# Kernel tuning notes

Measured on AMD Instinct MI355X. Metric: run time of the kernel, lower is better.

## Reference

```python
import jax, jax.numpy as jnp
import numpy as np

B, C, H, W = 2, 48, 64, 64
EPS = 1e-5
ROW = [0, 0, 0, H // 4, H // 4, H // 4, H // 2, H // 2, H // 2]
COL = [0, W // 4, W // 2] * 3


def setup_inputs() -> dict:
    key = jax.random.key(0)
    ks = iter(jax.random.split(key, 40))
    s = 1.0 / np.sqrt(C)  # keep unscaled-softmax logits sane
    def rn(shape, scale=1.0):
        return jax.random.normal(next(ks), shape, jnp.float32) * scale
    def ru(shape):
        return jax.random.uniform(next(ks), shape, jnp.float32, 0.5, 1.5)
    return dict(
        input_feature=rn((B, C, H, W)), feat_b=rn((B, C, H, W)),
        feat_c=rn((B, C, H, W)), feat_d=rn((B, C, H, W)),
        W_fa_all=rn((C, C), s), W_fb_all=rn((C, C), s),
        W_fc_all=rn((C, C), s), W_fd_all=rn((C, C), s),
        W_fa=rn((9, C, C), s), W_fb=rn((9, C, C), s),
        W_fc=rn((9, C, C), s), W_fd=rn((9, C, C), s),
        fuse_w=rn((C, 4 * C), s), fuse_b=rn((C,), 0.1),
        fuse_g=ru((C,)), fuse_bb=rn((C,), 0.1), fuse_m=rn((C,), 0.1), fuse_v=ru((C,)),
        fuseP_w=rn((9, C, 4 * C), s), fuseP_b=rn((9, C), 0.1),
        fuseP_g=ru((9, C)), fuseP_bb=rn((9, C), 0.1), fuseP_m=rn((9, C), 0.1), fuseP_v=ru((9, C)),
        gamma_all=rn(()), gamma_p=rn((9,)),
        out_w=rn((C, C, 3, 3), s / 3.0), out_b=rn((C,), 0.1),
        out_g=ru((C,)), out_bb=rn((C,), 0.1), out_m=rn((C,), 0.1), out_v=ru((C,)),
    )


def _attn(q, k, v):
    # q,k,v: [..., C, N] -> energy [..., N, N]; non-standard softmax(max - energy)
    e = jnp.einsum('...cn,...cm->...nm', q, k)
    e = jnp.max(e, axis=-1, keepdims=True) - e
    a = jax.nn.softmax(e, axis=-1)
    return jnp.einsum('...cn,...nm->...cm', v, a)  # torch.matmul(v, attention)


def reference(input_feature, feat_b, feat_c, feat_d,
              W_fa_all, W_fb_all, W_fc_all, W_fd_all,
              W_fa, W_fb, W_fc, W_fd,
              fuse_w, fuse_b, fuse_g, fuse_bb, fuse_m, fuse_v,
              fuseP_w, fuseP_b, fuseP_g, fuseP_bb, fuseP_m, fuseP_v,
              gamma_all, gamma_p,
              out_w, out_b, out_g, out_bb, out_m, out_v):
    h2, w2 = H // 2, W // 2
    N = H * W
    # ---- global branch: channel-wise Linear (bias=False) applied over spatial tokens
    fa = jnp.einsum('dc,bcn->bdn', W_fa_all, input_feature.reshape(B, C, N))
    fb = jnp.einsum('dc,bcn->bdn', W_fb_all, feat_b.reshape(B, C, N))
    fc = jnp.einsum('dc,bcn->bdn', W_fc_all, feat_c.reshape(B, C, N))
    fd = jnp.einsum('dc,bcn->bdn', W_fd_all, feat_d.reshape(B, C, N))
    cat = jnp.concatenate([_attn(fa, fa, fa), _attn(fa, fb, fb),
                           _attn(fa, fc, fc), _attn(fa, fd, fd)], axis=1)
    cat = cat.reshape(B, 4 * C, H, W)
    y = jnp.einsum('oc,bchw->bohw', fuse_w, cat) + fuse_b[None, :, None, None]
    y = (y - fuse_m[:, None, None]) * (fuse_g / jnp.sqrt(fuse_v + EPS))[:, None, None] + fuse_bb[:, None, None]
    atten_all = jax.nn.relu(y)  # Dropout2d is identity at eval
    # ---- 9 overlapping patch branches, vectorized over the patch axis p
    def crops(x):
        return jnp.stack([x[:, :, r:r + h2, c:c + w2] for r, c in zip(ROW, COL)], 0).reshape(9, B, C, h2 * w2)
    pa = jnp.einsum('pdc,pbcn->pbdn', W_fa, crops(input_feature))
    pb = jnp.einsum('pdc,pbcn->pbdn', W_fb, crops(feat_b))
    pc = jnp.einsum('pdc,pbcn->pbdn', W_fc, crops(feat_c))
    pd = jnp.einsum('pdc,pbcn->pbdn', W_fd, crops(feat_d))
    pcat = jnp.concatenate([_attn(pa, pa, pa), _attn(pa, pb, pb),
                            _attn(pa, pc, pc), _attn(pa, pd, pd)], axis=2)
    pcat = pcat.reshape(9, B, 4 * C, h2, w2)
    py = jnp.einsum('poc,pbchw->pbohw', fuseP_w, pcat) + fuseP_b[:, None, :, None, None]
    py = ((py - fuseP_m[:, None, :, None, None])
          * (fuseP_g / jnp.sqrt(fuseP_v + EPS))[:, None, :, None, None]
          + fuseP_bb[:, None, :, None, None])
    patch_out = 0.5 * gamma_p[:, None, None, None, None] * jax.nn.relu(py)
    # ---- combine (overlapping patch regions accumulate additively, as in torch +=)
    out = input_feature + gamma_all * atten_all
    for i, (r, c) in enumerate(zip(ROW, COL)):
        out = out.at[:, :, r:r + h2, c:c + w2].add(patch_out[i])
    # ---- to_out: 3x3 conv + BN(eval) + ReLU
    z = jax.lax.conv_general_dilated(out, out_w, (1, 1), 'SAME',
                                     dimension_numbers=('NCHW', 'OIHW', 'NCHW'))
    z = z + out_b[None, :, None, None]
    z = (z - out_m[:, None, None]) * (out_g / jnp.sqrt(out_v + EPS))[:, None, None] + out_bb[:, None, None]
    return jax.nn.relu(z)
```

## Files before the change

kernel.cpp:

```cpp
#include <hip/hip_runtime.h>
#include <math.h>

typedef _Float16 f16;
typedef f16 f16x8 __attribute__((ext_vector_type(8)));
typedef float f32x4 __attribute__((ext_vector_type(4)));

namespace {
constexpr int B_ = 2, C_ = 48, H_ = 64, W_ = 64;
constexpr int N_ = H_ * W_;
constexpr int NP_ = 1024;
constexpr int C4_ = 4 * C_;
constexpr float EPS_ = 1e-5f;
constexpr float L2E_ = 1.44269504f;
constexpr float REFL2_ = -25.0f * 1.44269504f;
}

#define MFMA32(a, b, c) __builtin_amdgcn_mfma_f32_16x16x32_f16((a), (b), (c), 0, 0, 0)

__device__ inline float fast_exp2(float x) {
#if __has_builtin(__builtin_amdgcn_exp2f)
  return __builtin_amdgcn_exp2f(x);
#else
  float r;
  asm("v_exp_f32 %0, %1" : "=v"(r) : "v"(x));
  return r;
#endif
}

__device__ __attribute__((always_inline)) void proj_body(
    const float* __restrict__ xb, const float* __restrict__ Ws,
    f16* __restrict__ pnb, size_t pn_stride, f16* __restrict__ ptb) {
  float acc[48];
#pragma unroll
  for (int d = 0; d < 48; ++d) acc[d] = 0.f;
  for (int c0 = 0; c0 < 48; c0 += 4) {
    float xv0 = xb[(size_t)(c0 + 0) * 4096];
    float xv1 = xb[(size_t)(c0 + 1) * 4096];
    float xv2 = xb[(size_t)(c0 + 2) * 4096];
    float xv3 = xb[(size_t)(c0 + 3) * 4096];
#pragma unroll
    for (int d = 0; d < 48; ++d) {
      const float4 wv = *(const float4*)&Ws[d * 48 + c0];
      acc[d] = fmaf(wv.x, xv0, fmaf(wv.y, xv1, fmaf(wv.z, xv2, fmaf(wv.w, xv3, acc[d]))));
    }
  }
#pragma unroll
  for (int d = 0; d < 48; ++d) pnb[(size_t)d * pn_stride] = (f16)acc[d];
#pragma unroll
  for (int s = 0; s < 6; ++s) {
    f16x8 v;
#pragma unroll
    for (int j = 0; j < 8; ++j) v[j] = (f16)acc[s * 8 + j];
    *(f16x8*)(ptb + s * 8) = v;
  }
  f16x8 zv = {0, 0, 0, 0, 0, 0, 0, 0};
  *(f16x8*)(ptb + 48) = zv;
  *(f16x8*)(ptb + 56) = zv;
}

__global__ __launch_bounds__(256) void k_proj_all(
    const float* __restrict__ x0, const float* __restrict__ x1,
    const float* __restrict__ x2, const float* __restrict__ x3,
    const float* __restrict__ w0, const float* __restrict__ w1,
    const float* __restrict__ w2, const float* __restrict__ w3,
    const float* __restrict__ wp0, const float* __restrict__ wp1,
    const float* __restrict__ wp2, const float* __restrict__ wp3,
    f16* __restrict__ pgn, f16* __restrict__ pgt,
    f16* __restrict__ ppn, f16* __restrict__ ppt) {
  __shared__ float Ws[48 * 48];
  int tid = threadIdx.x;
  int bid = blockIdx.x;
  if (bid < 128) {
    int bx = bid & 15, b = (bid >> 4) & 1, X = bid >> 5;
    const float* xp = X == 0 ? x0 : X == 1 ? x1 : X == 2 ? x2 : x3;
    const float* wp = X == 0 ? w0 : X == 1 ? w1 : X == 2 ? w2 : w3;
    for (int i = tid; i < 2304; i += 256) Ws[i] = wp[i];
    __syncthreads();
    int n = bx * 256 + tid;
    int z2 = X * 2 + b;
    proj_body(xp + (size_t)b * 48 * 4096 + n, Ws,
              pgn + ((size_t)z2 * 48) * 4096 + n, 4096,
              pgt + ((size_t)z2 * 4096 + n) * 64);
  } else {
    int pid = bid - 128;
    int bx = pid & 3;
    int rest = pid >> 2;
    int p = rest % 9;
    int zb = rest / 9;
    int X = zb >> 1, b = zb & 1;
    const float* xp = X == 0 ? x0 : X == 1 ? x1 : X == 2 ? x2 : x3;
    const float* wp = (X == 0 ? wp0 : X == 1 ? wp1 : X == 2 ? wp2 : wp3) + (size_t)p * 2304;
    for (int i = tid; i < 2304; i += 256) Ws[i] = wp[i];
    __syncthreads();
    int t = bx * 256 + tid;
    int r0 = (p / 3) * 16, c0w = (p % 3) * 16;
    int rr = r0 + (t >> 5), cc = c0w + (t & 31);
    int z9 = (X * 2 + b) * 9 + p;
    proj_body(xp + (size_t)b * 48 * 4096 + rr * 64 + cc, Ws,
              ppn + ((size_t)z9 * 48) * 1024 + t, 1024,
              ppt + ((size_t)z9 * 1024 + t) * 64);
  }
}

template <int NT, int NSPLIT, bool PATCH>
__device__ __attribute__((always_inline)) void stats_body(
    const f16* __restrict__ qT_all, const f16* __restrict__ kT_all,
    float* __restrict__ stp, int bx, int by, uint4* Ks) {
  constexpr int MTI = (NT / NSPLIT) / 64;
  int tid = threadIdx.x, wave = tid >> 6, lane = tid & 63, g = lane >> 4, lm = lane & 15;
  int ms = by % NSPLIT, z = by / NSPLIT;
  const f16* qT;
  if (PATCH) {
    int b = (z / 9) % 2, p = z % 9;
    qT = qT_all + ((size_t)(b * 9 + p)) * NT * 64;
  } else {
    int b = z & 1;
    qT = qT_all + (size_t)b * NT * 64;
  }
  const f16* kT = kT_all + (size_t)z * NT * 64;
  int n0 = bx * 128 + wave * 16;
  f16x8 aq0a = *(const f16x8*)(qT + (size_t)(n0 + lm) * 64 + g * 8);
  f16x8 aq1a = *(const f16x8*)(qT + (size_t)(n0 + lm) * 64 + 32 + g * 8);
  f16x8 aq0b = *(const f16x8*)(qT + (size_t)(n0 + 64 + lm) * 64 + g * 8);
  f16x8 aq1b = *(const f16x8*)(qT + (size_t)(n0 + 64 + lm) * 64 + 32 + g * 8);
  const int s0r = tid >> 3, s0c = (tid & 7) * 8;
  const int sw0 = tid ^ ((tid >> 3) & 7);
  const int sw1 = (tid + 256) ^ (((tid + 256) >> 3) & 7);
  const int swl = lm & 7;
  const int c0i = g ^ swl, c1i = (4 + g) ^ swl;
  int t_beg = ms * MTI;
  {
    const f16* src = kT + (size_t)t_beg * 64 * 64;
    Ks[sw0] = *(const uint4*)(src + (size_t)s0r * 64 + s0c);
    Ks[sw1] = *(const uint4*)(src + (size_t)(s0r + 32) * 64 + s0c);
  }
  __syncthreads();
  float zsa[4] = {0.f, 0.f, 0.f, 0.f};
  float zsb[4] = {0.f, 0.f, 0.f, 0.f};
  for (int mt = 0; mt < MTI; ++mt) {
    int cur = mt & 1;
    bool pf = (mt + 1 < MTI);
    uint4 k0v, k1v;
    if (pf) {
      const f16* src = kT + (size_t)(t_beg + mt + 1) * 64 * 64;
      k0v = *(const uint4*)(src + (size_t)s0r * 64 + s0c);
      k1v = *(const uint4*)(src + (size_t)(s0r + 32) * 64 + s0c);
    }
    uint4* kb = Ks + cur * 512;
    __builtin_amdgcn_s_setprio(1);
#pragma unroll
    for (int mf = 0; mf < 4; ++mf) {
      f16x8 b0 = __builtin_bit_cast(f16x8, kb[(16 * mf + lm) * 8 + c0i]);
      f16x8 b1 = __builtin_bit_cast(f16x8, kb[(16 * mf + lm) * 8 + c1i]);
      f32x4 ea = {0.f, 0.f, 0.f, 0.f};
      ea = MFMA32(aq0a, b0, ea);
      ea = MFMA32(aq1a, b1, ea);
      f32x4 eb = {0.f, 0.f, 0.f, 0.f};
      eb = MFMA32(aq0b, b0, eb);
      eb = MFMA32(aq1b, b1, eb);
#pragma unroll
      for (int r = 0; r < 4; ++r) {
        zsa[r] += fast_exp2(fmaf(ea[r], -L2E_, REFL2_));
        zsb[r] += fast_exp2(fmaf(eb[r], -L2E_, REFL2_));
      }
    }
    __builtin_amdgcn_s_setprio(0);
    if (pf) {
      uint4* kn = Ks + (cur ^ 1) * 512;
      kn[sw0] = k0v;
      kn[sw1] = k1v;
    }
    __syncthreads();
  }
#pragma unroll
  for (int mask = 1; mask < 16; mask <<= 1) {
#pragma unroll
    for (int r = 0; r < 4; ++r) {
      zsa[r] += __shfl_xor(zsa[r], mask, 64);
      zsb[r] += __shfl_xor(zsb[r], mask, 64);
    }
  }
  if (lm == 0) {
#pragma unroll
    for (int r = 0; r < 4; ++r) {
      stp[((size_t)z * NT + n0 + 4 * g + r) * NSPLIT + ms] = zsa[r];
      stp[((size_t)z * NT + n0 + 64 + 4 * g + r) * NSPLIT + ms] = zsb[r];
    }
  }
}

__global__ __launch_bounds__(256, 6) void k_stats_all(
    const f16* __restrict__ pg_t, float* __restrict__ stpg,
    const f16* __restrict__ pp_t, float* __restrict__ stpp) {
  __shared__ uint4 Ks[2 * 512];
  int bid = blockIdx.x;
  if (bid < 1024) {
    stats_body<N_, 4, false>(pg_t, pg_t, stpg, bid & 31, bid >> 5, Ks);
  } else {
    int pid = bid - 1024;
    stats_body<NP_, 1, true>(pp_t, pp_t, stpp, pid & 7, pid >> 3, Ks);
  }
}

__global__ __launch_bounds__(256) void k_merge_all(
    const float* __restrict__ stpg, float* __restrict__ stg,
    const float* __restrict__ stpp, float* __restrict__ stp2) {
  int i = blockIdx.x * 256 + threadIdx.x;
  if (i < 8 * N_) {
    const float* p = stpg + (size_t)i * 4;
    float Z = p[0] + p[1] + p[2] + p[3];
    stg[i] = REFL2_ - __log2f(Z);
  } else {
    int j = i - 8 * N_;
    if (j < 72 * NP_) stp2[j] = REFL2_ - __log2f(stpp[j]);
  }
}

template <int NT, int NSPLIT, bool PATCH>
__device__ __attribute__((always_inline)) void pv_body(
    const f16* __restrict__ qT_all, const f16* __restrict__ kT_all,
    const f16* __restrict__ vN_all, const float* __restrict__ st_all,
    float* __restrict__ out_all, int bx, int by,
    float* As2, uint4* Qs, uint4* Vs, uint2* wt2) {
  constexpr int CH = NT / NSPLIT;
  constexpr int NTI = CH / 64;
  int tid = threadIdx.x, wave = tid >> 6, lane = tid & 63, g = lane >> 4, lm = lane & 15;
  int ns = by % NSPLIT, z = by / NSPLIT;
  const f16 *qT, *kT, *vN;
  float* op;
  if (PATCH) {
    int X = z / 18, b = (z / 9) % 2, p = z % 9;
    qT = qT_all + ((size_t)(b * 9 + p)) * NT * 64;
    op = out_all + ((size_t)((p * 2 + b) * C4_ + X * 48)) * NT;
  } else {
    int X = z >> 1, b = z & 1;
    qT = qT_all + (size_t)b * NT * 64;
    op = out_all + ((size_t)(b * C4_ + X * 48)) * NT;
  }
  kT = kT_all + (size_t)z * NT * 64;
  vN = vN_all + (size_t)z * 48 * NT;
  const float* st = st_all + (size_t)z * NT + ns * CH;
  ((float4*)As2)[tid] = ((const float4*)st)[tid];
  int mwa = bx * 128 + wave * 16;
  int mwb = mwa + 64;
  f16x8 bk0a = *(const f16x8*)(kT + (size_t)(mwa + lm) * 64 + g * 8);
  f16x8 bk1a = *(const f16x8*)(kT + (size_t)(mwa + lm) * 64 + 32 + g * 8);
  f16x8 bk0b = *(const f16x8*)(kT + (size_t)(mwb + lm) * 64 + g * 8);
  f16x8 bk1b = *(const f16x8*)(kT + (size_t)(mwb + lm) * 64 + 32 + g * 8);
  const int s0r = tid >> 3, s0c = (tid & 7) * 8;
  const int sw0 = tid ^ ((tid >> 3) & 7);
  const int sw1 = (tid + 256) ^ (((tid + 256) >> 3) & 7);
  const int swl = lm & 7;
  const int c0i = g ^ swl, c1i = (4 + g) ^ swl;
  int t_beg = ns * NTI;
  {
    const f16* qsrc = qT + (size_t)t_beg * 64 * 64;
    Qs[sw0] = *(const uint4*)(qsrc + (size_t)s0r * 64 + s0c);
    Qs[sw1] = *(const uint4*)(qsrc + (size_t)(s0r + 32) * 64 + s0c);
    Vs[sw0] = *(const uint4*)(vN + (size_t)s0r * NT + t_beg * 64 + s0c);
    if (tid < 128)
      Vs[sw1] = *(const uint4*)(vN + (size_t)(s0r + 32) * NT + t_beg * 64 + s0c);
  }
  __syncthreads();
  f32x4 oa0 = {0.f, 0.f, 0.f, 0.f}, oa1 = {0.f, 0.f, 0.f, 0.f}, oa2 = {0.f, 0.f, 0.f, 0.f};
  f32x4 ob0 = {0.f, 0.f, 0.f, 0.f}, ob1 = {0.f, 0.f, 0.f, 0.f}, ob2 = {0.f, 0.f, 0.f, 0.f};
  int wbufa = wave * 512;
  int wbufb = wave * 512 + 256;
  int rba = wbufa + lm * 16;
  int rbb = wbufb + lm * 16;
  for (int nt = 0; nt < NTI; ++nt) {
    bool pf = (nt + 1 < NTI);
    uint4 q0v, q1v, v0v, v1v;
    if (pf) {
      int tn = t_beg + nt + 1;
      const f16* qsrc = qT + (size_t)tn * 64 * 64;
      q0v = *(const uint4*)(qsrc + (size_t)s0r * 64 + s0c);
      q1v = *(const uint4*)(qsrc + (size_t)(s0r + 32) * 64 + s0c);
      v0v = *(const uint4*)(vN + (size_t)s0r * NT + tn * 64 + s0c);
      if (tid < 128)
        v1v = *(const uint4*)(vN + (size_t)(s0r + 32) * NT + tn * 64 + s0c);
    }
    f32x4 ea[4], eb[4];
    __builtin_amdgcn_s_setprio(1);
#pragma unroll
    for (int nf = 0; nf < 4; ++nf) {
      f16x8 a0 = __builtin_bit_cast(f16x8, Qs[(16 * nf + lm) * 8 + c0i]);
      f16x8 a1 = __builtin_bit_cast(f16x8, Qs[(16 * nf + lm) * 8 + c1i]);
      f32x4 ta = {0.f, 0.f, 0.f, 0.f};
      ta = MFMA32(a0, bk0a, ta);
      ta = MFMA32(a1, bk1a, ta);
      ea[nf] = ta;
      f32x4 tb = {0.f, 0.f, 0.f, 0.f};
      tb = MFMA32(a0, bk0b, tb);
      tb = MFMA32(a1, bk1b, tb);
      eb[nf] = tb;
    }
    __builtin_amdgcn_s_setprio(0);
#pragma unroll
    for (int nf = 0; nf < 4; ++nf) {
      float4 a4 = *(const float4*)&As2[nt * 64 + nf * 16 + g * 4];
      float wa0 = fast_exp2(fmaf(ea[nf][0], -L2E_, a4.x));
      float wa1 = fast_exp2(fmaf(ea[nf][1], -L2E_, a4.y));
      float wa2 = fast_exp2(fmaf(ea[nf][2], -L2E_, a4.z));
      float wa3 = fast_exp2(fmaf(ea[nf][3], -L2E_, a4.w));
      float wb0 = fast_exp2(fmaf(eb[nf][0], -L2E_, a4.x));
      float wb1 = fast_exp2(fmaf(eb[nf][1], -L2E_, a4.y));
      float wb2 = fast_exp2(fmaf(eb[nf][2], -L2E_, a4.z));
      float wb3 = fast_exp2(fmaf(eb[nf][3], -L2E_, a4.w));
      unsigned la = __builtin_bit_cast(unsigned, __builtin_amdgcn_cvt_pkrtz(wa0, wa1));
      unsigned ha = __builtin_bit_cast(unsigned, __builtin_amdgcn_cvt_pkrtz(wa2, wa3));
      unsigned lb = __builtin_bit_cast(unsigned, __builtin_amdgcn_cvt_pkrtz(wb0, wb1));
      unsigned hb = __builtin_bit_cast(unsigned, __builtin_amdgcn_cvt_pkrtz(wb2, wb3));
      int s = 2 * nf + (g >> 1);
      int so = ((s ^ swl) * 2) + (g & 1);
      wt2[wbufa + lm * 16 + so] = make_uint2(la, ha);
      wt2[wbufb + lm * 16 + so] = make_uint2(lb, hb);
    }
    __builtin_amdgcn_sched_barrier(0);
    f16x8 bw0a = __builtin_bit_cast(f16x8, *(const uint4*)&wt2[rba + c0i * 2]);
    f16x8 bw1a = __builtin_bit_cast(f16x8, *(const uint4*)&wt2[rba + c1i * 2]);
    f16x8 bw0b = __builtin_bit_cast(f16x8, *(const uint4*)&wt2[rbb + c0i * 2]);
    f16x8 bw1b = __builtin_bit_cast(f16x8, *(const uint4*)&wt2[rbb + c1i * 2]);
    __builtin_amdgcn_s_setprio(1);
#pragma unroll
    for (int cf = 0; cf < 3; ++cf) {
      f16x8 av0 = __builtin_bit_cast(f16x8, Vs[(16 * cf + lm) * 8 + c0i]);
      f16x8 av1 = __builtin_bit_cast(f16x8, Vs[(16 * cf + lm) * 8 + c1i]);
      if (cf == 0) {
        oa0 = MFMA32(av0, bw0a, oa0); oa0 = MFMA32(av1, bw1a, oa0);
        ob0 = MFMA32(av0, bw0b, ob0); ob0 = MFMA32(av1, bw1b, ob0);
      }
      if (cf == 1) {
        oa1 = MFMA32(av0, bw0a, oa1); oa1 = MFMA32(av1, bw1a, oa1);
        ob1 = MFMA32(av0, bw0b, ob1); ob1 = MFMA32(av1, bw1b, ob1);
      }
      if (cf == 2) {
        oa2 = MFMA32(av0, bw0a, oa2); oa2 = MFMA32(av1, bw1a, oa2);
        ob2 = MFMA32(av0, bw0b, ob2); ob2 = MFMA32(av1, bw1b, ob2);
      }
    }
    __builtin_amdgcn_s_setprio(0);
    __syncthreads();
    if (pf) {
      Qs[sw0] = q0v;
      Qs[sw1] = q1v;
      Vs[sw0] = v0v;
      if (tid < 128) Vs[sw1] = v1v;
    }
    __syncthreads();
  }
  if (NSPLIT == 1) {
#pragma unroll
    for (int r = 0; r < 4; ++r) {
      op[(size_t)(0 + 4 * g + r) * NT + mwa + lm] = oa0[r];
      op[(size_t)(16 + 4 * g + r) * NT + mwa + lm] = oa1[r];
      op[(size_t)(32 + 4 * g + r) * NT + mwa + lm] = oa2[r];
      op[(size_t)(0 + 4 * g + r) * NT + mwb + lm] = ob0[r];
      op[(size_t)(16 + 4 * g + r) * NT + mwb + lm] = ob1[r];
      op[(size_t)(32 + 4 * g + r) * NT + mwb + lm] = ob2[r];
    }
  } else {
#pragma unroll
    for (int r = 0; r < 4; ++r) {
      atomicAdd(&op[(size_t)(0 + 4 * g + r) * NT + mwa + lm], oa0[r]);
      atomicAdd(&op[(size_t)(16 + 4 * g + r) * NT + mwa + lm], oa1[r]);
      atomicAdd(&op[(size_t)(32 + 4 * g + r) * NT + mwa + lm], oa2[r]);
      atomicAdd(&op[(size_t)(0 + 4 * g + r) * NT + mwb + lm], ob0[r]);
      atomicAdd(&op[(size_t)(16 + 4 * g + r) * NT + mwb + lm], ob1[r]);
      atomicAdd(&op[(size_t)(32 + 4 * g + r) * NT + mwb + lm], ob2[r]);
    }
  }
}

__global__ __launch_bounds__(256, 4) void k_pv_all(
    const f16* __restrict__ pg_t, const f16* __restrict__ pg_n,
    const float* __restrict__ statsg, float* __restrict__ cat,
    const f16* __restrict__ pp_t, const f16* __restrict__ pp_n,
    const float* __restrict__ statsp, float* __restrict__ pcat) {
  __shared__ float As2[1024];
  __shared__ uint4 Qs[512];
  __shared__ uint4 Vs[384];
  __shared__ uint2 wt2[2048];
  int bid = blockIdx.x;
  if (bid < 1024) {
    pv_body<N_, 4, false>(pg_t, pg_t, pg_n, statsg, cat, bid & 31, bid >> 5,
                          As2, Qs, Vs, wt2);
  } else {
    int pid = bid - 1024;
    pv_body<NP_, 1, true>(pp_t, pp_t, pp_n, statsp, pcat, pid & 7, pid >> 3,
                          As2, Qs, Vs, wt2);
  }
}

__global__ __launch_bounds__(256) void k_fuse_all(
    const float* __restrict__ cat, const float* __restrict__ fw,
    const float* __restrict__ fb, const float* __restrict__ fg,
    const float* __restrict__ fbb, const float* __restrict__ fm,
    const float* __restrict__ fv, const float* __restrict__ gamma_all,
    const float* __restrict__ input, float* __restrict__ comb,
    const float* __restrict__ pcat, const float* __restrict__ pfw,
    const float* __restrict__ pfb, const float* __restrict__ pfg,
    const float* __restrict__ pfbb, const float* __restrict__ pfm,
    const float* __restrict__ pfv, const float* __restrict__ gamma_p) {
  int bid = blockIdx.x;
  if (bid < 384) {
    int idx = bid * 256 + threadIdx.x;
    int n4 = idx & 1023;
    int rest = idx >> 10;
    int o = rest % C_;
    int b = rest / C_;
    const float* cr = cat + (size_t)b * C4_ * N_ + n4 * 4;
    const float* wr = fw + (size_t)o * C4_;
    float4 acc = {0.f, 0.f, 0.f, 0.f};
#pragma unroll 8
    for (int c = 0; c < C4_; ++c) {
      float4 xv = *(const float4*)(cr + (size_t)c * N_);
      float w = wr[c];
      acc.x = fmaf(w, xv.x, acc.x); acc.y = fmaf(w, xv.y, acc.y);
      acc.z = fmaf(w, xv.z, acc.z); acc.w = fmaf(w, xv.w, acc.w);
    }
    float scale = fg[o] * rsqrtf(fv[o] + EPS_);
    float sh = fb[o] - fm[o], bb = fbb[o], ga = gamma_all[0];
    float4 inv = *(const float4*)(input + ((size_t)(b * C_ + o) * N_) + n4 * 4);
    float* base = comb + ((size_t)(b * C_ + o) * N_) + n4 * 4;
    atomicAdd(base + 0, inv.x + ga * fmaxf((acc.x + sh) * scale + bb, 0.f));
    atomicAdd(base + 1, inv.y + ga * fmaxf((acc.y + sh) * scale + bb, 0.f));
    atomicAdd(base + 2, inv.z + ga * fmaxf((acc.z + sh) * scale + bb, 0.f));
    atomicAdd(base + 3, inv.w + ga * fmaxf((acc.w + sh) * scale + bb, 0.f));
  } else {
    int idx = (bid - 384) * 256 + threadIdx.x;
    int t4 = idx & 255;
    int rest = idx >> 8;
    int o = rest % C_; rest /= C_;
    int b = rest % B_;
    int p = rest / B_;
    const float* cr = pcat + ((size_t)(p * B_ + b) * C4_) * NP_ + t4 * 4;
    const float* wr = pfw + (size_t)(p * C_ + o) * C4_;
    float4 acc = {0.f, 0.f, 0.f, 0.f};
#pragma unroll 8
    for (int c = 0; c < C4_; ++c) {
      float4 xv = *(const float4*)(cr + (size_t)c * NP_);
      float w = wr[c];
      acc.x = fmaf(w, xv.x, acc.x); acc.y = fmaf(w, xv.y, acc.y);
      acc.z = fmaf(w, xv.z, acc.z); acc.w = fmaf(w, xv.w, acc.w);
    }
    int po = p * C_ + o;
    float scale = pfg[po] * rsqrtf(pfv[po] + EPS_);
    float sh = pfb[po] - pfm[po], bb = pfbb[po], gp = 0.5f * gamma_p[p];
    int t = t4 * 4;
    int r0 = (p / 3) * 16, c0w = (p % 3) * 16;
    int h = r0 + (t >> 5), w = c0w + (t & 31);
    float* base = comb + ((size_t)(b * C_ + o) * N_) + h * 64 + w;
    atomicAdd(base + 0, gp * fmaxf((acc.x + sh) * scale + bb, 0.f));
    atomicAdd(base + 1, gp * fmaxf((acc.y + sh) * scale + bb, 0.f));
    atomicAdd(base + 2, gp * fmaxf((acc.z + sh) * scale + bb, 0.f));
    atomicAdd(base + 3, gp * fmaxf((acc.w + sh) * scale + bb, 0.f));
  }
}

__global__ __launch_bounds__(256) void k_conv2(
    const float* __restrict__ comb, const float* __restrict__ cw,
    const float* __restrict__ cb, const float* __restrict__ cg,
    const float* __restrict__ cbb, const float* __restrict__ cm,
    const float* __restrict__ cv, float* __restrict__ out) {
  __shared__ float4 inh[4608];
  int tid = threadIdx.x;
  int h0 = blockIdx.x * 4, ocg = blockIdx.y, b = blockIdx.z;
  for (int i = tid; i < 4608; i += 256) {
    int c = i / 96;
    int rem = i - c * 96;
    int r = rem >> 4, u = rem & 15;
    int hh = h0 - 1 + r;
    float4 val = make_float4(0.f, 0.f, 0.f, 0.f);
    if (hh >= 0 && hh < H_)
      val = *(const float4*)(comb + (((size_t)(b * C_ + c) * H_ + hh) * W_ + u * 4));
    inh[i] = val;
  }
  __syncthreads();
  int w = tid & 63, dh = tid >> 6;
  float acc[6] = {0.f, 0.f, 0.f, 0.f, 0.f, 0.f};
  const float* lds = (const float*)inh;
  int wm = w > 0 ? w - 1 : 0;
  int wp = w < 63 ? w + 1 : 63;
  for (int c = 0; c < 48; ++c) {
    float v[9];
#pragma unroll
    for (int r = 0; r < 3; ++r) {
      const float* row = lds + (size_t)(c * 6 + dh + r) * 64;
      float lf = row[wm];
      float md = row[w];
      float rt = row[wp];
      v[r * 3 + 0] = (w > 0) ? lf : 0.f;
      v[r * 3 + 1] = md;
      v[r * 3 + 2] = (w < 63) ? rt : 0.f;
    }
#pragma unroll
    for (int j = 0; j < 6; ++j) {
      const float* wr = cw + (size_t)((ocg * 6 + j) * 48 + c) * 9;
#pragma unroll
      for (int k = 0; k < 9; ++k) acc[j] = fmaf(v[k], wr[k], acc[j]);
    }
  }
#pragma unroll
  for (int j = 0; j < 6; ++j) {
    int o = ocg * 6 + j;
    float scale = cg[o] * rsqrtf(cv[o] + EPS_);
    float y = (acc[j] + cb[o] - cm[o]) * scale + cbb[o];
    out[(size_t)(b * C_ + o) * N_ + (h0 + dh) * 64 + w] = fmaxf(y, 0.f);
  }
}

extern "C" void kernel_launch(void* const* d_in, const int* in_sizes, int n_in,
                              void* d_out, int out_size, void* d_ws, size_t ws_size,
                              hipStream_t stream) {
  (void)in_sizes; (void)n_in; (void)out_size; (void)ws_size;
  const float* x[4];
  const float* Wall[4];
  const float* Wp[4];
  for (int i = 0; i < 4; ++i) {
    x[i] = (const float*)d_in[i];
    Wall[i] = (const float*)d_in[4 + i];
    Wp[i] = (const float*)d_in[8 + i];
  }
  const float* fuse_w = (const float*)d_in[12];
  const float* fuse_b = (const float*)d_in[13];
  const float* fuse_g = (const float*)d_in[14];
  const float* fuse_bb = (const float*)d_in[15];
  const float* fuse_m = (const float*)d_in[16];
  const float* fuse_v = (const float*)d_in[17];
  const float* fuseP_w = (const float*)d_in[18];
  const float* fuseP_b = (const float*)d_in[19];
  const float* fuseP_g = (const float*)d_in[20];
  const float* fuseP_bb = (const float*)d_in[21];
  const float* fuseP_m = (const float*)d_in[22];
  const float* fuseP_v = (const float*)d_in[23];
  const float* gamma_all = (const float*)d_in[24];
  const float* gamma_p = (const float*)d_in[25];
  const float* out_w = (const float*)d_in[26];
  const float* out_b = (const float*)d_in[27];
  const float* out_g = (const float*)d_in[28];
  const float* out_bb = (const float*)d_in[29];
  const float* out_m = (const float*)d_in[30];
  const float* out_v = (const float*)d_in[31];

  char* base = (char*)d_ws;
  size_t off = 0;
  auto carve = [&](size_t bytes) {
    char* p = base + off;
    off += (bytes + 255) & ~(size_t)255;
    return p;
  };
  f16* projg_n = (f16*)carve((size_t)8 * 48 * N_ * 2);
  f16* projg_t = (f16*)carve((size_t)8 * N_ * 64 * 2);
  f16* projp_n = (f16*)carve((size_t)72 * 48 * NP_ * 2);
  f16* projp_t = (f16*)carve((size_t)72 * NP_ * 64 * 2);
  float* stpg = (float*)carve((size_t)8 * N_ * 4 * 4);
  float* stpp = (float*)carve((size_t)72 * NP_ * 4);
  float* statsg = (float*)carve((size_t)8 * N_ * 4);
  float* statsp = (float*)carve((size_t)72 * NP_ * 4);
  float* cat = (float*)carve((size_t)B_ * C4_ * N_ * 4);
  float* pcat = (float*)carve((size_t)9 * B_ * C4_ * NP_ * 4);
  float* comb = (float*)carve((size_t)B_ * C_ * N_ * 4);

  dim3 blk(256);

  (void)hipMemsetAsync(cat, 0, (size_t)B_ * C4_ * N_ * sizeof(float), stream);
  (void)hipMemsetAsync(comb, 0, (size_t)B_ * C_ * N_ * sizeof(float), stream);
  k_proj_all<<<dim3(416), blk, 0, stream>>>(
      x[0], x[1], x[2], x[3], Wall[0], Wall[1], Wall[2], Wall[3],
      Wp[0], Wp[1], Wp[2], Wp[3], projg_n, projg_t, projp_n, projp_t);

  k_stats_all<<<dim3(1600), blk, 0, stream>>>(projg_t, stpg, projp_t, stpp);
  k_merge_all<<<dim3((8 * N_ + 72 * NP_ + 255) / 256), blk, 0, stream>>>(
      stpg, statsg, stpp, statsp);

  k_pv_all<<<dim3(1600), blk, 0, stream>>>(
      projg_t, projg_n, statsg, cat, projp_t, projp_n, statsp, pcat);

  k_fuse_all<<<dim3(1248), blk, 0, stream>>>(
      cat, fuse_w, fuse_b, fuse_g, fuse_bb, fuse_m, fuse_v, gamma_all, x[0], comb,
      pcat, fuseP_w, fuseP_b, fuseP_g, fuseP_bb, fuseP_m, fuseP_v, gamma_p);
  k_conv2<<<dim3(16, 8, 2), blk, 0, stream>>>(
      comb, out_w, out_b, out_g, out_bb, out_m, out_v, (float*)d_out);
}
```

Measured before the change: 240.7 us.

## Stage fuse-conv input panel in LDS and compute 12 outputs per thread

Rewrites the 1x1 fuse kernels so each block loads a 192x64 panel of the concatenated attention output into shared memory once. Each thread then computes 12 output channels for one spatial position, instead of every output channel re-reading the full input column from global memory. This cuts redundant global traffic on the cat/pcat tensors and shrinks the grid from 1248 to 416 blocks. In exchange, atomics are now scalar rather than 4-wide, weights are read per-k from global (broadcast across the wave), and fewer blocks are in flight.

```diff
diff --git a/kernel.cpp b/kernel.cpp
--- a/kernel.cpp
+++ b/kernel.cpp
@@ -392,7 +392,7 @@
   }
 }
 
-__global__ __launch_bounds__(256) void k_fuse_all(
+__global__ __launch_bounds__(256) void k_fuse2(
     const float* __restrict__ cat, const float* __restrict__ fw,
     const float* __restrict__ fb, const float* __restrict__ fg,
     const float* __restrict__ fbb, const float* __restrict__ fm,
@@ -402,59 +402,67 @@
     const float* __restrict__ pfb, const float* __restrict__ pfg,
     const float* __restrict__ pfbb, const float* __restrict__ pfm,
     const float* __restrict__ pfv, const float* __restrict__ gamma_p) {
+  __shared__ float panel[192 * 64];
+  int tid = threadIdx.x;
   int bid = blockIdx.x;
-  if (bid < 384) {
-    int idx = bid * 256 + threadIdx.x;
-    int n4 = idx & 1023;
-    int rest = idx >> 10;
-    int o = rest % C_;
-    int b = rest / C_;
-    const float* cr = cat + (size_t)b * C4_ * N_ + n4 * 4;
-    const float* wr = fw + (size_t)o * C4_;
-    float4 acc = {0.f, 0.f, 0.f, 0.f};
-#pragma unroll 8
+  int n = tid & 63, og = tid >> 6;
+  if (bid < 128) {
+    int b = bid >> 6;
+    int n0 = (bid & 63) * 64;
+    const float* src = cat + (size_t)b * C4_ * N_ + n0;
+    for (int i = tid; i < 3072; i += 256) {
+      int c = i >> 4, j = (i & 15) * 4;
+      *(float4*)&panel[c * 64 + j] = *(const float4*)(src + (size_t)c * N_ + j);
+    }
+    __syncthreads();
+    float acc[12] = {0.f, 0.f, 0.f, 0.f, 0.f, 0.f, 0.f, 0.f, 0.f, 0.f, 0.f, 0.f};
+    const float* wbase = fw + (size_t)(og * 12) * C4_;
     for (int c = 0; c < C4_; ++c) {
-      float4 xv = *(const float4*)(cr + (size_t)c * N_);
-      float w = wr[c];
-      acc.x = fmaf(w, xv.x, acc.x); acc.y = fmaf(w, xv.y, acc.y);
-      acc.z = fmaf(w, xv.z, acc.z); acc.w = fmaf(w, xv.w, acc.w);
-    }
-    float scale = fg[o] * rsqrtf(fv[o] + EPS_);
-    float sh = fb[o] - fm[o], bb = fbb[o], ga = gamma_all[0];
-    float4 inv = *(const float4*)(input + ((size_t)(b * C_ + o) * N_) + n4 * 4);
-    float* base = comb + ((size_t)(b * C_ + o) * N_) + n4 * 4;
-    atomicAdd(base + 0, inv.x + ga * fmaxf((acc.x + sh) * scale + bb, 0.f));
-    atomicAdd(base + 1, inv.y + ga * fmaxf((acc.y + sh) * scale + bb, 0.f));
-    atomicAdd(base + 2, inv.z + ga * fmaxf((acc.z + sh) * scale + bb, 0.f));
-    atomicAdd(base + 3, inv.w + ga * fmaxf((acc.w + sh) * scale + bb, 0.f));
-  } else {
-    int idx = (bid - 384) * 256 + threadIdx.x;
-    int t4 = idx & 255;
-    int rest = idx >> 8;
-    int o = rest % C_; rest /= C_;
-    int b = rest % B_;
-    int p = rest / B_;
-    const float* cr = pcat + ((size_t)(p * B_ + b) * C4_) * NP_ + t4 * 4;
-    const float* wr = pfw + (size_t)(p * C_ + o) * C4_;
-    float4 acc = {0.f, 0.f, 0.f, 0.f};
-#pragma unroll 8
+      float xv = panel[c * 64 + n];
+#pragma unroll
+      for (int k = 0; k < 12; ++k)
+        acc[k] = fmaf(wbase[(size_t)k * C4_ + c], xv, acc[k]);
+    }
+    float ga = gamma_all[0];
+#pragma unroll
+    for (int k = 0; k < 12; ++k) {
+      int o = og * 12 + k;
+      float scale = fg[o] * rsqrtf(fv[o] + EPS_);
+      float y = (acc[k] + fb[o] - fm[o]) * scale + fbb[o];
+      size_t oi = ((size_t)(b * C_ + o)) * N_ + n0 + n;
+      atomicAdd(&comb[oi], input[oi] + ga * fmaxf(y, 0.f));
+    }
+  } else {
+    int pid = bid - 128;
+    int slice = pid >> 4;
+    int t0 = (pid & 15) * 64;
+    int p = slice >> 1, b = slice & 1;
+    const float* src = pcat + (size_t)slice * C4_ * NP_ + t0;
+    for (int i = tid; i < 3072; i += 256) {
+      int c = i >> 4, j = (i & 15) * 4;
+      *(float4*)&panel[c * 64 + j] = *(const float4*)(src + (size_t)c * NP_ + j);
+    }
+    __syncthreads();
+    float acc[12] = {0.f, 0.f, 0.f, 0.f, 0.f, 0.f, 0.f, 0.f, 0.f, 0.f, 0.f, 0.f};
+    const float* wbase = pfw + ((size_t)p * C_ + og * 12) * C4_;
     for (int c = 0; c < C4_; ++c) {
-      float4 xv = *(const float4*)(cr + (size_t)c * NP_);
-      float w = wr[c];
-      acc.x = fmaf(w, xv.x, acc.x); acc.y = fmaf(w, xv.y, acc.y);
-      acc.z = fmaf(w, xv.z, acc.z); acc.w = fmaf(w, xv.w, acc.w);
-    }
-    int po = p * C_ + o;
-    float scale = pfg[po] * rsqrtf(pfv[po] + EPS_);
-    float sh = pfb[po] - pfm[po], bb = pfbb[po], gp = 0.5f * gamma_p[p];
-    int t = t4 * 4;
+      float xv = panel[c * 64 + n];
+#pragma unroll
+      for (int k = 0; k < 12; ++k)
+        acc[k] = fmaf(wbase[(size_t)k * C4_ + c], xv, acc[k]);
+    }
+    int t = t0 + n;
     int r0 = (p / 3) * 16, c0w = (p % 3) * 16;
     int h = r0 + (t >> 5), w = c0w + (t & 31);
-    float* base = comb + ((size_t)(b * C_ + o) * N_) + h * 64 + w;
-    atomicAdd(base + 0, gp * fmaxf((acc.x + sh) * scale + bb, 0.f));
-    atomicAdd(base + 1, gp * fmaxf((acc.y + sh) * scale + bb, 0.f));
-    atomicAdd(base + 2, gp * fmaxf((acc.z + sh) * scale + bb, 0.f));
-    atomicAdd(base + 3, gp * fmaxf((acc.w + sh) * scale + bb, 0.f));
+    float gp = 0.5f * gamma_p[p];
+#pragma unroll
+    for (int k = 0; k < 12; ++k) {
+      int o = og * 12 + k;
+      int po = p * C_ + o;
+      float scale = pfg[po] * rsqrtf(pfv[po] + EPS_);
+      float y = (acc[k] + pfb[po] - pfm[po]) * scale + pfbb[po];
+      atomicAdd(&comb[((size_t)(b * C_ + o)) * N_ + h * 64 + w], gp * fmaxf(y, 0.f));
+    }
   }
 }
 
@@ -577,7 +585,7 @@
   k_pv_all<<<dim3(1600), blk, 0, stream>>>(
       projg_t, projg_n, statsg, cat, projp_t, projp_n, statsp, pcat);
 
-  k_fuse_all<<<dim3(1248), blk, 0, stream>>>(
+  k_fuse2<<<dim3(416), blk, 0, stream>>>(
       cat, fuse_w, fuse_b, fuse_g, fuse_bb, fuse_m, fuse_v, gamma_all, x[0], comb,
       pcat, fuseP_w, fuseP_b, fuseP_g, fuseP_bb, fuseP_m, fuseP_v, gamma_p);
   k_conv2<<<dim3(16, 8, 2), blk, 0, stream>>>(
```

Result: faster. 233.0 us (median of 2 runs) (-3.2%).
